# Optimization experiments

Measured on AMD Instinct MI355X. Metric: run time of the kernel, lower is better.

The kernel has to match this reference:

```python
import jax, jax.numpy as jnp
import numpy as np

DEPTH = 3

def _rx(theta):
    c, s = jnp.cos(theta / 2), jnp.sin(theta / 2)
    return jnp.stack([jnp.stack([c + 0j, -1j * s], -1),
                      jnp.stack([-1j * s, c + 0j], -1)], -2)

def _ry(theta):
    c, s = jnp.cos(theta / 2), jnp.sin(theta / 2)
    return jnp.stack([jnp.stack([c + 0j, -s + 0j], -1),
                      jnp.stack([s + 0j, c + 0j], -1)], -2)

def _rz(theta):
    e = jnp.exp(-0.5j * theta.astype(jnp.complex64))
    z = jnp.zeros_like(e)
    return jnp.stack([jnp.stack([e, z], -1),
                      jnp.stack([z, jnp.conj(e)], -1)], -2)

def _apply_1q(state, U, q):
    # state: (batch, 2,2,...,2); wire q lives on axis q+1. U: (2,2) or (batch,2,2)
    s = jnp.moveaxis(state, q + 1, -1)
    if U.ndim == 3:
        s = jnp.einsum('b...i,bji->b...j', s, U)
    else:
        s = jnp.einsum('...i,ji->...j', s, U)
    return jnp.moveaxis(s, -1, q + 1)

def _apply_cnot(state, c, t):
    s = jnp.moveaxis(state, (c + 1, t + 1), (-2, -1))
    s = jnp.concatenate([s[..., 0:1, :], s[..., 1:2, ::-1]], axis=-2)
    return jnp.moveaxis(s, (-2, -1), (c + 1, t + 1))

def _circuit(x, params):
    batch, n = x.shape
    depth = params.shape[0]
    state = jnp.zeros((batch,) + (2,) * n, jnp.complex64)
    state = state.at[(slice(None),) + (0,) * n].set(1.0)
    # data-encoding RX with per-sample angles
    for q in range(n):
        state = _apply_1q(state, _rx(x[:, q].astype(jnp.complex64).real), q)
    for l in range(depth):
        for q in range(n):
            state = _apply_1q(state, _rx(params[l, q, 0]), q)
            state = _apply_1q(state, _ry(params[l, q, 1]), q)
            state = _apply_1q(state, _rz(params[l, q, 2]), q)
        for q in range(n - 1):
            state = _apply_cnot(state, q, q + 1)
        state = _apply_cnot(state, n - 1, 0)
    probs = state.real ** 2 + state.imag ** 2  # (batch, 2,...,2)
    exps = []
    for w in range(n):
        p = jnp.moveaxis(probs, w + 1, 1).reshape(batch, 2, -1).sum(-1)
        exps.append(p[:, 0] - p[:, 1])  # <Z_w> = P(0) - P(1)
    return jnp.stack(exps, axis=1)


def setup_inputs() -> dict:
    key = jax.random.key(0)
    k1, k2 = jax.random.split(key)
    batch, n = 128, 14
    x = jax.random.normal(k1, (batch, n), dtype=jnp.float32)
    params = jax.random.normal(k2, (DEPTH, n, 3), dtype=jnp.float32)
    return {"x": x, "params": params}


def reference(x, params):
    return _circuit(x, params)
```

## Files before the change

kernel.cpp:

```cpp
#include <hip/hip_runtime.h>

namespace {

constexpr int NQ      = 14;
constexpr int NSTATES = 1 << NQ;
constexpr int BLOCK   = 1024;
constexpr int NWAVES  = BLOCK / 64;

constexpr unsigned cparity(unsigned x){ x^=x>>8; x^=x>>4; x^=x>>2; x^=x>>1; return x&1u; }

struct Mat { unsigned row[NQ]; unsigned col[NQ]; };

constexpr Mat m_after(int nr){
  Mat m{};
  for(int p=0;p<NQ;++p){ m.row[p]=1u<<p; m.col[p]=1u<<p; }
  for(int l=0;l<nr;++l)
    for(int q=0;q<NQ;++q){
      int cq=(q==NQ-1)?NQ-1:q, tq=(q==NQ-1)?0:q+1;
      int Pc=NQ-1-cq, Pt=NQ-1-tq;
      m.row[Pt]^=m.row[Pc]; m.col[Pc]^=m.col[Pt];
    }
  return m;
}

constexpr Mat M1=m_after(1), M2=m_after(2), M3=m_after(3);
constexpr unsigned amask(int q){ return M1.col[NQ-1-q]; }
constexpr unsigned arow (int q){ return M1.row[NQ-1-q]; }
constexpr unsigned bmask(int q){ return M2.col[NQ-1-q]; }
constexpr unsigned brow (int q){ return M2.row[NQ-1-q]; }

constexpr int rank_of(const unsigned* v, int n){
  unsigned a[24]{};
  for(int i=0;i<n;++i) a[i]=v[i];
  int r=0;
  for(int bit=15;bit>=0;--bit){
    int p=-1;
    for(int i=r;i<n;++i){ if((a[i]>>bit)&1){ p=i; break; } }
    if(p<0) continue;
    unsigned t=a[r]; a[r]=a[p]; a[p]=t;
    for(int i=0;i<n;++i) if(i!=r && ((a[i]>>bit)&1)) a[i]^=a[r];
    ++r;
  }
  return r;
}

struct Plan {
  unsigned A[14], B[14], C[14];
  int BlaneGi[6]; unsigned BlanePi4[6];
  int BregGi[4];  unsigned BregEps[4];
  int CregGi[4];  unsigned CregEps[4];
  int ClaneGi[4]; unsigned ClaneEps[4];
  unsigned EJ4[14], ET[14];
};

constexpr Plan make_plan(){
  Plan P{};
  for(int t=0;t<14;++t) P.A[t]=amask(t);
  for(int t=0;t<4;++t){ P.B[t]=amask(10+t); P.BregGi[t]=10+t; }
  bool used[14]{}; int picked[14]{}; int np=0;
  {
    unsigned cur[20]{}; int nc=0;
    for(int t=0;t<4;++t) cur[nc++]=P.B[t];
    for(int q=0;q<14 && np<10;++q){
      cur[nc]=bmask(q);
      if(rank_of(cur,nc+1)==nc+1){ ++nc; picked[np++]=q; used[q]=true; }
    }
  }
  for(int i=0;i<6;++i){ P.B[4+i]=bmask(picked[i]); P.BlaneGi[i]=14+picked[i]; }
  int wq[4]{}, un[4]{}; int nu=0;
  for(int i=0;i<4;++i){ wq[i]=picked[6+i]; P.B[10+i]=bmask(wq[i]); P.CregGi[i]=14+wq[i]; }
  for(int q=0;q<14;++q) if(!used[q]) un[nu++]=q;
  for(int i=0;i<4;++i) P.ClaneGi[i]=14+un[i];
  for(int i=0;i<4;++i){ unsigned m=0;
    for(int t=0;t<10;++t) m |= cparity(arow(10+i)&P.B[4+t])<<t;
    P.BregEps[i]=m; }
  for(int i=0;i<6;++i){ unsigned m=0;
    for(int t=0;t<4;++t) m |= cparity(brow(picked[i])&P.B[t])<<t;
    P.BlanePi4[i]=m; }
  for(int t=0;t<4;++t) P.C[t]=bmask(wq[t]);
  for(int t=0;t<4;++t) P.C[4+t]=bmask(un[t]);
  {
    unsigned cc[20]{}; int n=0;
    for(int t=0;t<8;++t) cc[n++]=P.C[t];
    int pos=8;
    for(int p=0;p<14 && pos<14;++p){
      cc[n]=1u<<p;
      if(rank_of(cc,n+1)==n+1){ P.C[pos]=1u<<p; ++n; ++pos; }
    }
  }
  for(int i=0;i<4;++i){ unsigned m=0;
    for(int t=0;t<10;++t) m |= cparity(brow(wq[i])&P.C[4+t])<<t;
    P.CregEps[i]=m; }
  for(int i=0;i<4;++i){ unsigned m=0;
    for(int t=0;t<10;++t){ if(t==i) continue; m |= cparity(brow(un[i])&P.C[4+t])<<t; }
    P.ClaneEps[i]=m; }
  for(int w=0;w<14;++w){
    unsigned R=M3.row[NQ-1-w]; unsigned mj=0, mt=0;
    for(int t=0;t<4;++t)  mj |= cparity(R&P.C[t])<<t;
    for(int t=0;t<10;++t) mt |= cparity(R&P.C[4+t])<<t;
    P.EJ4[w]=mj; P.ET[w]=mt;
  }
  return P;
}

constexpr Plan PL = make_plan();
static_assert(rank_of(PL.A,14)==14, "phase A map not bijective");
static_assert(rank_of(PL.B,14)==14, "phase B map not bijective");
static_assert(rank_of(PL.C,14)==14, "phase C map not bijective");

struct Inv { unsigned col[NQ]; };
constexpr Inv inv_basis(const unsigned* bas){
  unsigned vec[NQ]{}, cmb[NQ]{}; bool used[NQ]{}; int pivk[NQ]{};
  for(int k=0;k<NQ;++k){ vec[k]=bas[k]; cmb[k]=1u<<k; }
  for(int b=0;b<NQ;++b){
    int p=-1;
    for(int k=0;k<NQ;++k) if(!used[k] && ((vec[k]>>b)&1)){ p=k; break; }
    used[p]=true; pivk[b]=p;
    for(int k=0;k<NQ;++k) if(k!=p && ((vec[k]>>b)&1)){ vec[k]^=vec[p]; cmb[k]^=cmb[p]; }
  }
  Inv R{};
  for(int b=0;b<NQ;++b) R.col[b]=cmb[pivk[b]];
  return R;
}
constexpr bool check_inv(const unsigned* bas, const Inv& iv){
  for(int p=0;p<NQ;++p){
    unsigned s=0;
    for(int k=0;k<NQ;++k) if((iv.col[p]>>k)&1) s^=bas[k];
    if(s != (1u<<p)) return false;
  }
  return true;
}
constexpr Inv IA = inv_basis(PL.A), IB = inv_basis(PL.B), IC = inv_basis(PL.C);
static_assert(check_inv(PL.A, IA), "IA");
static_assert(check_inv(PL.B, IB), "IB");
static_assert(check_inv(PL.C, IC), "IC");

struct Trans { unsigned t[NQ]; };
constexpr Trans trans_phys(const Inv& iv){
  Trans T{};
  for(int p=0;p<NQ;++p) T.t[p]=iv.col[p];
  return T;
}
constexpr Trans trans_of(const unsigned* cur, const Inv& iv){
  Trans T{};
  for(int k=0;k<NQ;++k){
    unsigned c=0;
    for(int p=0;p<NQ;++p) if((cur[k]>>p)&1) c^=iv.col[p];
    T.t[k]=c;
  }
  return T;
}
constexpr Trans T_PA = trans_phys(IA);
constexpr Trans T_AB = trans_of(PL.A, IB);
constexpr Trans T_BC = trans_of(PL.B, IC);

struct CJ { unsigned v[16]; };
constexpr CJ mk_cj(const Trans& T){
  CJ c{};
  for(int j=0;j<16;++j){
    unsigned s=0;
    for(int b=0;b<4;++b) if((j>>b)&1) s^=T.t[b];
    c.v[j]=s;
  }
  return c;
}
constexpr CJ CJ_PA=mk_cj(T_PA), CJ_AB=mk_cj(T_AB), CJ_BC=mk_cj(T_BC);

__device__ __forceinline__ float2 cmul2(float2 a, float2 b){
  return make_float2(fmaf(a.x, b.x, -(a.y * b.y)),
                     fmaf(a.x, b.y,  a.y * b.x));
}
__device__ __forceinline__ float2 cfma2(float2 a, float2 b, float2 c){
  return make_float2(fmaf(a.x, b.x, fmaf(-a.y, b.y, c.x)),
                     fmaf(a.x, b.y, fmaf( a.y, b.x, c.y)));
}
__device__ __forceinline__ float2 sel2f(bool c, float2 x, float2 y){
  return make_float2(c ? x.x : y.x, c ? x.y : y.y);
}

struct GC { float2 u00,u01,u10,u11; };
__device__ __forceinline__ GC load_gc(const float2* __restrict__ g){
  const float4* p = reinterpret_cast<const float4*>(g);
  float4 q0=p[0], q1=p[1];
  GC c;
  c.u00=make_float2(q0.x,q0.y); c.u01=make_float2(q0.z,q0.w);
  c.u10=make_float2(q1.x,q1.y); c.u11=make_float2(q1.z,q1.w);
  return c;
}

template<int CTRL>
__device__ __forceinline__ int dpp(int x){
  return __builtin_amdgcn_update_dpp(0, x, CTRL, 0xF, 0xF, true);
}
__device__ __forceinline__ int x32(int x, unsigned lane){
  auto r = __builtin_amdgcn_permlane32_swap((unsigned)x, (unsigned)x, false, false);
  return (lane & 32u) ? (int)r[0] : (int)r[1];
}
template<int K>
__device__ __forceinline__ float2 xpart(float2 v, unsigned lane){
  int x0=__float_as_int(v.x), x1=__float_as_int(v.y);
  int y0, y1;
  if constexpr (K==0){ y0=dpp<0xB1>(x0);  y1=dpp<0xB1>(x1); }
  else if constexpr (K==1){ y0=dpp<0x4E>(x0);  y1=dpp<0x4E>(x1); }
  else if constexpr (K==2){
    y0=__builtin_amdgcn_ds_swizzle(x0,0x101F);
    y1=__builtin_amdgcn_ds_swizzle(x1,0x101F);
  }
  else if constexpr (K==3){ y0=dpp<0x128>(x0); y1=dpp<0x128>(x1); }
  else if constexpr (K==4){
    y0=__builtin_amdgcn_ds_swizzle(x0,0x401F);
    y1=__builtin_amdgcn_ds_swizzle(x1,0x401F);
  }
  else { y0=x32(x0,lane); y1=x32(x1,lane); }
  return make_float2(__int_as_float(y0), __int_as_float(y1));
}

template<int BIT>
__device__ __forceinline__ void reg_gate(float2 (&a)[16], const GC& c, bool eps){
  float2 m00=sel2f(eps,c.u11,c.u00), m01=sel2f(eps,c.u10,c.u01);
  float2 m10=sel2f(eps,c.u01,c.u10), m11=sel2f(eps,c.u00,c.u11);
#pragma unroll
  for(int v=0; v<16; ++v){
    if(!((v>>BIT)&1)){
      int w = v | (1<<BIT);
      float2 a0=a[v], a1=a[w];
      a[v] = cfma2(m01, a1, cmul2(m00, a0));
      a[w] = cfma2(m11, a1, cmul2(m10, a0));
    }
  }
}

template<int XK, unsigned PI4>
__device__ __forceinline__ void lane_gate(float2 (&a)[16], const GC& c, bool sel, unsigned lane){
  float2 ka0=sel2f(sel,c.u11,c.u00), kb0=sel2f(sel,c.u10,c.u01);
  float2 ka1=sel2f(sel,c.u00,c.u11), kb1=sel2f(sel,c.u01,c.u10);
  float2 th[16];
#pragma unroll
  for(int j=0;j<16;++j) th[j] = xpart<XK>(a[j], lane);
#pragma unroll
  for(int j=0;j<16;++j){
    bool pi = (__builtin_popcount(PI4 & (unsigned)j) & 1) != 0;
    float2 ka = pi?ka1:ka0, kb = pi?kb1:kb0;
    a[j] = cfma2(kb, th[j], cmul2(ka, a[j]));
  }
}

__device__ __forceinline__ unsigned nb_of(unsigned tid, const unsigned (&t)[NQ]){
  unsigned s=0;
#pragma unroll
  for(int k=0;k<10;++k) s ^= t[4+k] & (0u-((tid>>k)&1u));
  return s;
}

__device__ __forceinline__ void scatter16(float2* __restrict__ st, const float2 (&a)[16],
                                          unsigned nb, const CJ& cj){
#pragma unroll
  for(int j=0;j<16;++j){
    unsigned d = nb ^ cj.v[j];
    st[d + (d>>4)] = a[j];
  }
}

__global__ __launch_bounds__(BLOCK, 4) void qsim_kernel(
    const float* __restrict__ x,
    const float* __restrict__ prm,
    float* __restrict__ out)
{
  __shared__ float2 st[BLOCK*17];
  __shared__ alignas(16) float2 Utab[28*4];
  __shared__ float2 l0c[NQ][2];
  __shared__ float  red[NWAVES][NQ];

  const int b = blockIdx.x;
  const unsigned tid = threadIdx.x;
  const unsigned lane = tid & 63u;

  if(tid < 28){
    int t = tid;
    int l = 1 + t/NQ, q = t % NQ;
    float ax=prm[(l*NQ+q)*3+0], ay=prm[(l*NQ+q)*3+1], az=prm[(l*NQ+q)*3+2];
    float cx,sx,cy,sy,cz,sz;
    sincosf(0.5f*ax,&sx,&cx); sincosf(0.5f*ay,&sy,&cy); sincosf(0.5f*az,&sz,&cz);
    float2 M00=make_float2(cy*cx, sy*sx),  M01=make_float2(-sy*cx,-cy*sx);
    float2 M10=make_float2(sy*cx,-cy*sx),  M11=make_float2(cy*cx,-sy*sx);
    float2 ez =make_float2(cz,-sz), ezc=make_float2(cz,sz);
    float2* U = &Utab[t*4];
    U[0]=cmul2(ez,M00); U[1]=cmul2(ez,M01);
    U[2]=cmul2(ezc,M10); U[3]=cmul2(ezc,M11);
  }
  if(tid < NQ){
    int q = tid;
    float ax = prm[q*3+0] + x[b*NQ+q];
    float ay = prm[q*3+1], az = prm[q*3+2];
    float cx,sx,cy,sy,cz,sz;
    sincosf(0.5f*ax,&sx,&cx); sincosf(0.5f*ay,&sy,&cy); sincosf(0.5f*az,&sz,&cz);
    l0c[q][0] = cmul2(make_float2(cz,-sz), make_float2(cy*cx,  sy*sx));
    l0c[q][1] = cmul2(make_float2(cz, sz), make_float2(sy*cx, -cy*sx));
  }
  __syncthreads();

  {
    float2 p01 = cmul2(l0c[0][(tid>>9)&1],  l0c[1][(tid>>8)&1]);
    float2 p23 = cmul2(l0c[2][(tid>>7)&1],  l0c[3][(tid>>6)&1]);
    float2 p45 = cmul2(l0c[4][(tid>>5)&1],  l0c[5][(tid>>4)&1]);
    float2 p67 = cmul2(l0c[6][(tid>>3)&1],  l0c[7][(tid>>2)&1]);
    float2 p89 = cmul2(l0c[8][(tid>>1)&1],  l0c[9][tid&1]);
    float2 Pk  = cmul2(cmul2(cmul2(p01,p23), cmul2(p45,p67)), p89);
    float2 t2[2], t4[4];
    t2[0]=cmul2(Pk,l0c[10][0]); t2[1]=cmul2(Pk,l0c[10][1]);
#pragma unroll
    for(int i=0;i<2;++i){ t4[2*i]=cmul2(t2[i],l0c[11][0]); t4[2*i+1]=cmul2(t2[i],l0c[11][1]); }
    float2 a[16];
#pragma unroll
    for(int j=0;j<16;++j){
      a[j] = cmul2(cmul2(t4[j>>2], l0c[12][(j>>1)&1]), l0c[13][j&1]);
    }
    scatter16(st, a, nb_of(tid, T_PA.t), CJ_PA);
  }
  __syncthreads();

  {
    float2 a[16];
    const int rb = (int)tid*17;
#pragma unroll
    for(int j=0;j<16;++j) a[j] = st[rb + j];
    reg_gate<0>(a, load_gc(Utab+0*4), false);
    reg_gate<1>(a, load_gc(Utab+1*4), false);
    reg_gate<2>(a, load_gc(Utab+2*4), false);
    reg_gate<3>(a, load_gc(Utab+3*4), false);
    lane_gate<0,0u>(a, load_gc(Utab+4*4), (tid&1)!=0,  lane);
    lane_gate<1,0u>(a, load_gc(Utab+5*4), (tid&2)!=0,  lane);
    lane_gate<2,0u>(a, load_gc(Utab+6*4), (tid&4)!=0,  lane);
    lane_gate<3,0u>(a, load_gc(Utab+7*4), (tid&8)!=0,  lane);
    lane_gate<4,0u>(a, load_gc(Utab+8*4), (tid&16)!=0, lane);
    lane_gate<5,0u>(a, load_gc(Utab+9*4), (tid&32)!=0, lane);
    __syncthreads();
    scatter16(st, a, nb_of(tid, T_AB.t), CJ_AB);
  }
  __syncthreads();

  {
    float2 a[16];
    const int rb = (int)tid*17;
#pragma unroll
    for(int j=0;j<16;++j) a[j] = st[rb + j];
    reg_gate<0>(a, load_gc(Utab+PL.BregGi[0]*4), (__builtin_popcount(PL.BregEps[0]&tid)&1)!=0);
    reg_gate<1>(a, load_gc(Utab+PL.BregGi[1]*4), (__builtin_popcount(PL.BregEps[1]&tid)&1)!=0);
    reg_gate<2>(a, load_gc(Utab+PL.BregGi[2]*4), (__builtin_popcount(PL.BregEps[2]&tid)&1)!=0);
    reg_gate<3>(a, load_gc(Utab+PL.BregGi[3]*4), (__builtin_popcount(PL.BregEps[3]&tid)&1)!=0);
    lane_gate<0,PL.BlanePi4[0]>(a, load_gc(Utab+PL.BlaneGi[0]*4), (tid&1)!=0,  lane);
    lane_gate<1,PL.BlanePi4[1]>(a, load_gc(Utab+PL.BlaneGi[1]*4), (tid&2)!=0,  lane);
    lane_gate<2,PL.BlanePi4[2]>(a, load_gc(Utab+PL.BlaneGi[2]*4), (tid&4)!=0,  lane);
    lane_gate<3,PL.BlanePi4[3]>(a, load_gc(Utab+PL.BlaneGi[3]*4), (tid&8)!=0,  lane);
    lane_gate<4,PL.BlanePi4[4]>(a, load_gc(Utab+PL.BlaneGi[4]*4), (tid&16)!=0, lane);
    lane_gate<5,PL.BlanePi4[5]>(a, load_gc(Utab+PL.BlaneGi[5]*4), (tid&32)!=0, lane);
    __syncthreads();
    scatter16(st, a, nb_of(tid, T_BC.t), CJ_BC);
  }
  __syncthreads();

  {
    float2 a[16];
    const int rb = (int)tid*17;
#pragma unroll
    for(int j=0;j<16;++j) a[j] = st[rb + j];
    reg_gate<0>(a, load_gc(Utab+PL.CregGi[0]*4), (__builtin_popcount(PL.CregEps[0]&tid)&1)!=0);
    reg_gate<1>(a, load_gc(Utab+PL.CregGi[1]*4), (__builtin_popcount(PL.CregEps[1]&tid)&1)!=0);
    reg_gate<2>(a, load_gc(Utab+PL.CregGi[2]*4), (__builtin_popcount(PL.CregEps[2]&tid)&1)!=0);
    reg_gate<3>(a, load_gc(Utab+PL.CregGi[3]*4), (__builtin_popcount(PL.CregEps[3]&tid)&1)!=0);
    lane_gate<0,0u>(a, load_gc(Utab+PL.ClaneGi[0]*4),
        (((tid&1u)!=0) != ((__builtin_popcount(PL.ClaneEps[0]&tid)&1)!=0)), lane);
    lane_gate<1,0u>(a, load_gc(Utab+PL.ClaneGi[1]*4),
        (((tid&2u)!=0) != ((__builtin_popcount(PL.ClaneEps[1]&tid)&1)!=0)), lane);
    lane_gate<2,0u>(a, load_gc(Utab+PL.ClaneGi[2]*4),
        (((tid&4u)!=0) != ((__builtin_popcount(PL.ClaneEps[2]&tid)&1)!=0)), lane);
    lane_gate<3,0u>(a, load_gc(Utab+PL.ClaneGi[3]*4),
        (((tid&8u)!=0) != ((__builtin_popcount(PL.ClaneEps[3]&tid)&1)!=0)), lane);

    float p[16];
#pragma unroll
    for(int j=0;j<16;++j) p[j] = a[j].x*a[j].x + a[j].y*a[j].y;
#pragma unroll
    for(int bstep=1; bstep<16; bstep<<=1){
#pragma unroll
      for(int j=0;j<16;++j){
        if(!(j & bstep)){
          float u = p[j], v = p[j|bstep];
          p[j] = u + v;
          p[j|bstep] = u - v;
        }
      }
    }
    const int wave = tid >> 6;
#pragma unroll
    for(int w=0;w<NQ;++w){
      float v = (__builtin_popcount(PL.ET[w]&tid)&1) ? -p[PL.EJ4[w]] : p[PL.EJ4[w]];
#pragma unroll
      for(int off=32; off>0; off>>=1) v += __shfl_down(v, off, 64);
      if(lane==0) red[wave][w]=v;
    }
    __syncthreads();
    if(tid < NQ){
      float s=0.f;
#pragma unroll
      for(int wv=0; wv<NWAVES; ++wv) s += red[wv][tid];
      out[b*NQ + tid] = s;
    }
  }
}

}

extern "C" void kernel_launch(void* const* d_in, const int* in_sizes, int n_in,
                              void* d_out, int out_size, void* d_ws, size_t ws_size,
                              hipStream_t stream) {
  const float* x   = (const float*)d_in[0];
  const float* prm = (const float*)d_in[1];
  float* out = (float*)d_out;
  const int batch = in_sizes[0] / NQ;
  qsim_kernel<<<batch, BLOCK, 0, stream>>>(x, prm, out);
}
```

Measured before the change: 37.97 us.

## Store state in LDS as packed fp16, use permlane16 swap and DPP reductions

The shared-memory state buffer changes from float2 to packed half2 (cvt_pkrtz on write, convert back on read). This halves LDS footprint and bandwidth per scatter and gather, and the smaller buffer could also let more blocks fit per CU. The lane-16 exchange now uses permlane16_swap instead of ds_swizzle where the builtin exists. The wave reduction is rewritten from shfl_down to a DPP, swizzle and permlane butterfly. Storing amplitudes in fp16 between stages lowers precision and risks accuracy tolerance failures.

```diff
diff --git a/kernel.cpp b/kernel.cpp
--- a/kernel.cpp
+++ b/kernel.cpp
@@ -166,6 +166,16 @@
 }
 constexpr CJ CJ_PA=mk_cj(T_PA), CJ_AB=mk_cj(T_AB), CJ_BC=mk_cj(T_BC);
 
+using h2v = __fp16 __attribute__((ext_vector_type(2)));
+__device__ __forceinline__ unsigned pack_h2(float2 a){
+  h2v h = __builtin_amdgcn_cvt_pkrtz(a.x, a.y);
+  return __builtin_bit_cast(unsigned, h);
+}
+__device__ __forceinline__ float2 unpack_h2(unsigned u){
+  h2v h = __builtin_bit_cast(h2v, u);
+  return make_float2((float)h[0], (float)h[1]);
+}
+
 __device__ __forceinline__ float2 cmul2(float2 a, float2 b){
   return make_float2(fmaf(a.x, b.x, -(a.y * b.y)),
                      fmaf(a.x, b.y,  a.y * b.x));
@@ -195,6 +205,14 @@
 __device__ __forceinline__ int x32(int x, unsigned lane){
   auto r = __builtin_amdgcn_permlane32_swap((unsigned)x, (unsigned)x, false, false);
   return (lane & 32u) ? (int)r[0] : (int)r[1];
+}
+__device__ __forceinline__ int x16(int x, unsigned lane){
+#if __has_builtin(__builtin_amdgcn_permlane16_swap)
+  auto r = __builtin_amdgcn_permlane16_swap((unsigned)x, (unsigned)x, false, false);
+  return (lane & 16u) ? (int)r[0] : (int)r[1];
+#else
+  return __builtin_amdgcn_ds_swizzle(x, 0x401F);
+#endif
 }
 template<int K>
 __device__ __forceinline__ float2 xpart(float2 v, unsigned lane){
@@ -207,10 +225,7 @@
     y1=__builtin_amdgcn_ds_swizzle(x1,0x101F);
   }
   else if constexpr (K==3){ y0=dpp<0x128>(x0); y1=dpp<0x128>(x1); }
-  else if constexpr (K==4){
-    y0=__builtin_amdgcn_ds_swizzle(x0,0x401F);
-    y1=__builtin_amdgcn_ds_swizzle(x1,0x401F);
-  }
+  else if constexpr (K==4){ y0=x16(x0,lane); y1=x16(x1,lane); }
   else { y0=x32(x0,lane); y1=x32(x1,lane); }
   return make_float2(__int_as_float(y0), __int_as_float(y1));
 }
@@ -245,6 +260,16 @@
   }
 }
 
+__device__ __forceinline__ float xsum64(float v, unsigned lane){
+  v += __int_as_float(dpp<0xB1>(__float_as_int(v)));
+  v += __int_as_float(dpp<0x4E>(__float_as_int(v)));
+  v += __int_as_float(__builtin_amdgcn_ds_swizzle(__float_as_int(v),0x101F));
+  v += __int_as_float(dpp<0x128>(__float_as_int(v)));
+  v += __int_as_float(x16(__float_as_int(v), lane));
+  v += __int_as_float(x32(__float_as_int(v), lane));
+  return v;
+}
+
 __device__ __forceinline__ unsigned nb_of(unsigned tid, const unsigned (&t)[NQ]){
   unsigned s=0;
 #pragma unroll
@@ -252,12 +277,12 @@
   return s;
 }
 
-__device__ __forceinline__ void scatter16(float2* __restrict__ st, const float2 (&a)[16],
+__device__ __forceinline__ void scatter16(unsigned* __restrict__ st, const float2 (&a)[16],
                                           unsigned nb, const CJ& cj){
 #pragma unroll
   for(int j=0;j<16;++j){
     unsigned d = nb ^ cj.v[j];
-    st[d + (d>>4)] = a[j];
+    st[d + (d>>4)] = pack_h2(a[j]);
   }
 }
 
@@ -266,7 +291,7 @@
     const float* __restrict__ prm,
     float* __restrict__ out)
 {
-  __shared__ float2 st[BLOCK*17];
+  __shared__ unsigned st[BLOCK*17];
   __shared__ alignas(16) float2 Utab[28*4];
   __shared__ float2 l0c[NQ][2];
   __shared__ float  red[NWAVES][NQ];
@@ -323,7 +348,7 @@
     float2 a[16];
     const int rb = (int)tid*17;
 #pragma unroll
-    for(int j=0;j<16;++j) a[j] = st[rb + j];
+    for(int j=0;j<16;++j) a[j] = unpack_h2(st[rb + j]);
     reg_gate<0>(a, load_gc(Utab+0*4), false);
     reg_gate<1>(a, load_gc(Utab+1*4), false);
     reg_gate<2>(a, load_gc(Utab+2*4), false);
@@ -343,7 +368,7 @@
     float2 a[16];
     const int rb = (int)tid*17;
 #pragma unroll
-    for(int j=0;j<16;++j) a[j] = st[rb + j];
+    for(int j=0;j<16;++j) a[j] = unpack_h2(st[rb + j]);
     reg_gate<0>(a, load_gc(Utab+PL.BregGi[0]*4), (__builtin_popcount(PL.BregEps[0]&tid)&1)!=0);
     reg_gate<1>(a, load_gc(Utab+PL.BregGi[1]*4), (__builtin_popcount(PL.BregEps[1]&tid)&1)!=0);
     reg_gate<2>(a, load_gc(Utab+PL.BregGi[2]*4), (__builtin_popcount(PL.BregEps[2]&tid)&1)!=0);
@@ -363,7 +388,7 @@
     float2 a[16];
     const int rb = (int)tid*17;
 #pragma unroll
-    for(int j=0;j<16;++j) a[j] = st[rb + j];
+    for(int j=0;j<16;++j) a[j] = unpack_h2(st[rb + j]);
     reg_gate<0>(a, load_gc(Utab+PL.CregGi[0]*4), (__builtin_popcount(PL.CregEps[0]&tid)&1)!=0);
     reg_gate<1>(a, load_gc(Utab+PL.CregGi[1]*4), (__builtin_popcount(PL.CregEps[1]&tid)&1)!=0);
     reg_gate<2>(a, load_gc(Utab+PL.CregGi[2]*4), (__builtin_popcount(PL.CregEps[2]&tid)&1)!=0);
@@ -395,8 +420,7 @@
 #pragma unroll
     for(int w=0;w<NQ;++w){
       float v = (__builtin_popcount(PL.ET[w]&tid)&1) ? -p[PL.EJ4[w]] : p[PL.EJ4[w]];
-#pragma unroll
-      for(int off=32; off>0; off>>=1) v += __shfl_down(v, off, 64);
+      v = xsum64(v, lane);
       if(lane==0) red[wave][w]=v;
     }
     __syncthreads();
```

Result: slower. 43.56 us (+14.7%).

## Simulate state vector in packed half2 with fp16 FMA gates

Applied to the files above, without the earlier changes.

Stores the amplitudes as packed half2 (re, im) in registers and shared memory, and applies gates with packed fp16 FMAs. The gate coefficients are pre-expanded into duplicated half2 pairs, with a halfword swap for the cross terms. This halves LDS traffic and footprint and shrinks register pressure. Lane shuffles move one dword per amplitude instead of two. It also replaces the shfl_down reduction with a DPP/swizzle/permlane butterfly and uses permlane16_swap when it is available. The risk is fp16 precision loss across about 60 gate applications, which could exceed the accuracy tolerance.

```diff
diff --git a/kernel.cpp b/kernel.cpp
--- a/kernel.cpp
+++ b/kernel.cpp
@@ -1,4 +1,5 @@
 #include <hip/hip_runtime.h>
+#include <hip/hip_fp16.h>
 
 namespace {
 
@@ -166,83 +167,102 @@
 }
 constexpr CJ CJ_PA=mk_cj(T_PA), CJ_AB=mk_cj(T_AB), CJ_BC=mk_cj(T_BC);
 
+__device__ __forceinline__ __half2 H2(unsigned u){ return __builtin_bit_cast(__half2, u); }
+__device__ __forceinline__ unsigned U32(__half2 h){ return __builtin_bit_cast(unsigned, h); }
+__device__ __forceinline__ unsigned hswap(unsigned u){ return __builtin_amdgcn_alignbit(u, u, 16); }
+
 __device__ __forceinline__ float2 cmul2(float2 a, float2 b){
   return make_float2(fmaf(a.x, b.x, -(a.y * b.y)),
                      fmaf(a.x, b.y,  a.y * b.x));
 }
-__device__ __forceinline__ float2 cfma2(float2 a, float2 b, float2 c){
-  return make_float2(fmaf(a.x, b.x, fmaf(-a.y, b.y, c.x)),
-                     fmaf(a.x, b.y, fmaf( a.y, b.x, c.y)));
-}
-__device__ __forceinline__ float2 sel2f(bool c, float2 x, float2 y){
-  return make_float2(c ? x.x : y.x, c ? x.y : y.y);
-}
-
-struct GC { float2 u00,u01,u10,u11; };
-__device__ __forceinline__ GC load_gc(const float2* __restrict__ g){
-  const float4* p = reinterpret_cast<const float4*>(g);
-  float4 q0=p[0], q1=p[1];
+
+struct GC { unsigned e[8]; };
+__device__ __forceinline__ GC load_gc(const unsigned* __restrict__ g){
+  const uint4* p = reinterpret_cast<const uint4*>(g);
+  uint4 q0=p[0], q1=p[1];
   GC c;
-  c.u00=make_float2(q0.x,q0.y); c.u01=make_float2(q0.z,q0.w);
-  c.u10=make_float2(q1.x,q1.y); c.u11=make_float2(q1.z,q1.w);
+  c.e[0]=q0.x; c.e[1]=q0.y; c.e[2]=q0.z; c.e[3]=q0.w;
+  c.e[4]=q1.x; c.e[5]=q1.y; c.e[6]=q1.z; c.e[7]=q1.w;
   return c;
 }
 
+__device__ __forceinline__ void gpair(__half2& r0, __half2& r1, const unsigned (&m)[8],
+                                      __half2 a0, __half2 a1){
+  __half2 a0s = H2(hswap(U32(a0))), a1s = H2(hswap(U32(a1)));
+  r0 = __hfma2(H2(m[0]),a0, __hfma2(H2(m[1]),a0s, __hfma2(H2(m[2]),a1, __hmul2(H2(m[3]),a1s))));
+  r1 = __hfma2(H2(m[4]),a0, __hfma2(H2(m[5]),a0s, __hfma2(H2(m[6]),a1, __hmul2(H2(m[7]),a1s))));
+}
+
 template<int CTRL>
-__device__ __forceinline__ int dpp(int x){
-  return __builtin_amdgcn_update_dpp(0, x, CTRL, 0xF, 0xF, true);
-}
-__device__ __forceinline__ int x32(int x, unsigned lane){
-  auto r = __builtin_amdgcn_permlane32_swap((unsigned)x, (unsigned)x, false, false);
-  return (lane & 32u) ? (int)r[0] : (int)r[1];
+__device__ __forceinline__ unsigned dppu(unsigned x){
+  return (unsigned)__builtin_amdgcn_update_dpp(0, (int)x, CTRL, 0xF, 0xF, true);
+}
+__device__ __forceinline__ unsigned x32u(unsigned x, unsigned lane){
+  auto r = __builtin_amdgcn_permlane32_swap(x, x, false, false);
+  return (lane & 32u) ? (unsigned)r[0] : (unsigned)r[1];
+}
+__device__ __forceinline__ unsigned x16u(unsigned x, unsigned lane){
+#if __has_builtin(__builtin_amdgcn_permlane16_swap)
+  auto r = __builtin_amdgcn_permlane16_swap(x, x, false, false);
+  return (lane & 16u) ? (unsigned)r[0] : (unsigned)r[1];
+#else
+  return (unsigned)__builtin_amdgcn_ds_swizzle((int)x, 0x401F);
+#endif
 }
 template<int K>
-__device__ __forceinline__ float2 xpart(float2 v, unsigned lane){
-  int x0=__float_as_int(v.x), x1=__float_as_int(v.y);
-  int y0, y1;
-  if constexpr (K==0){ y0=dpp<0xB1>(x0);  y1=dpp<0xB1>(x1); }
-  else if constexpr (K==1){ y0=dpp<0x4E>(x0);  y1=dpp<0x4E>(x1); }
-  else if constexpr (K==2){
-    y0=__builtin_amdgcn_ds_swizzle(x0,0x101F);
-    y1=__builtin_amdgcn_ds_swizzle(x1,0x101F);
-  }
-  else if constexpr (K==3){ y0=dpp<0x128>(x0); y1=dpp<0x128>(x1); }
-  else if constexpr (K==4){
-    y0=__builtin_amdgcn_ds_swizzle(x0,0x401F);
-    y1=__builtin_amdgcn_ds_swizzle(x1,0x401F);
-  }
-  else { y0=x32(x0,lane); y1=x32(x1,lane); }
-  return make_float2(__int_as_float(y0), __int_as_float(y1));
+__device__ __forceinline__ unsigned xpart_u32(unsigned x, unsigned lane){
+  if constexpr (K==0) return dppu<0xB1>(x);
+  else if constexpr (K==1) return dppu<0x4E>(x);
+  else if constexpr (K==2) return (unsigned)__builtin_amdgcn_ds_swizzle((int)x,0x101F);
+  else if constexpr (K==3) return dppu<0x128>(x);
+  else if constexpr (K==4) return x16u(x,lane);
+  else return x32u(x,lane);
 }
 
 template<int BIT>
-__device__ __forceinline__ void reg_gate(float2 (&a)[16], const GC& c, bool eps){
-  float2 m00=sel2f(eps,c.u11,c.u00), m01=sel2f(eps,c.u10,c.u01);
-  float2 m10=sel2f(eps,c.u01,c.u10), m11=sel2f(eps,c.u00,c.u11);
+__device__ __forceinline__ void reg_gate(__half2 (&a)[16], const GC& c, bool eps){
+  unsigned m[8];
+#pragma unroll
+  for(int i=0;i<8;++i) m[i] = eps ? c.e[i^6] : c.e[i];
 #pragma unroll
   for(int v=0; v<16; ++v){
     if(!((v>>BIT)&1)){
       int w = v | (1<<BIT);
-      float2 a0=a[v], a1=a[w];
-      a[v] = cfma2(m01, a1, cmul2(m00, a0));
-      a[w] = cfma2(m11, a1, cmul2(m10, a0));
+      __half2 n0, n1;
+      gpair(n0, n1, m, a[v], a[w]);
+      a[v]=n0; a[w]=n1;
     }
   }
 }
 
 template<int XK, unsigned PI4>
-__device__ __forceinline__ void lane_gate(float2 (&a)[16], const GC& c, bool sel, unsigned lane){
-  float2 ka0=sel2f(sel,c.u11,c.u00), kb0=sel2f(sel,c.u10,c.u01);
-  float2 ka1=sel2f(sel,c.u00,c.u11), kb1=sel2f(sel,c.u01,c.u10);
-  float2 th[16];
-#pragma unroll
-  for(int j=0;j<16;++j) th[j] = xpart<XK>(a[j], lane);
+__device__ __forceinline__ void lane_gate(__half2 (&a)[16], const GC& c, bool sel, unsigned lane){
+  unsigned ka0x = sel?c.e[6]:c.e[0], ka0n = sel?c.e[7]:c.e[1];
+  unsigned kb0x = sel?c.e[4]:c.e[2], kb0n = sel?c.e[5]:c.e[3];
+  unsigned ka1x = sel?c.e[0]:c.e[6], ka1n = sel?c.e[1]:c.e[7];
+  unsigned kb1x = sel?c.e[2]:c.e[4], kb1n = sel?c.e[3]:c.e[5];
+  unsigned th[16];
+#pragma unroll
+  for(int j=0;j<16;++j) th[j] = xpart_u32<XK>(U32(a[j]), lane);
 #pragma unroll
   for(int j=0;j<16;++j){
     bool pi = (__builtin_popcount(PI4 & (unsigned)j) & 1) != 0;
-    float2 ka = pi?ka1:ka0, kb = pi?kb1:kb0;
-    a[j] = cfma2(kb, th[j], cmul2(ka, a[j]));
-  }
+    unsigned kax = pi?ka1x:ka0x, kan = pi?ka1n:ka0n;
+    unsigned kbx = pi?kb1x:kb0x, kbn = pi?kb1n:kb0n;
+    __half2 as  = H2(hswap(U32(a[j])));
+    __half2 ths = H2(hswap(th[j]));
+    a[j] = __hfma2(H2(kax),a[j], __hfma2(H2(kan),as, __hfma2(H2(kbx),H2(th[j]), __hmul2(H2(kbn),ths))));
+  }
+}
+
+__device__ __forceinline__ float xsum64(float v, unsigned lane){
+  v += __int_as_float((int)dppu<0xB1>((unsigned)__float_as_int(v)));
+  v += __int_as_float((int)dppu<0x4E>((unsigned)__float_as_int(v)));
+  v += __int_as_float(__builtin_amdgcn_ds_swizzle(__float_as_int(v),0x101F));
+  v += __int_as_float((int)dppu<0x128>((unsigned)__float_as_int(v)));
+  v += __int_as_float((int)x16u((unsigned)__float_as_int(v), lane));
+  v += __int_as_float((int)x32u((unsigned)__float_as_int(v), lane));
+  return v;
 }
 
 __device__ __forceinline__ unsigned nb_of(unsigned tid, const unsigned (&t)[NQ]){
@@ -252,12 +272,12 @@
   return s;
 }
 
-__device__ __forceinline__ void scatter16(float2* __restrict__ st, const float2 (&a)[16],
+__device__ __forceinline__ void scatter16(unsigned* __restrict__ st, const __half2 (&a)[16],
                                           unsigned nb, const CJ& cj){
 #pragma unroll
   for(int j=0;j<16;++j){
     unsigned d = nb ^ cj.v[j];
-    st[d + (d>>4)] = a[j];
+    st[d + (d>>4)] = U32(a[j]);
   }
 }
 
@@ -266,8 +286,8 @@
     const float* __restrict__ prm,
     float* __restrict__ out)
 {
-  __shared__ float2 st[BLOCK*17];
-  __shared__ alignas(16) float2 Utab[28*4];
+  __shared__ unsigned st[BLOCK*17];
+  __shared__ alignas(16) unsigned Utab[28*8];
   __shared__ float2 l0c[NQ][2];
   __shared__ float  red[NWAVES][NQ];
 
@@ -284,9 +304,12 @@
     float2 M00=make_float2(cy*cx, sy*sx),  M01=make_float2(-sy*cx,-cy*sx);
     float2 M10=make_float2(sy*cx,-cy*sx),  M11=make_float2(cy*cx,-sy*sx);
     float2 ez =make_float2(cz,-sz), ezc=make_float2(cz,sz);
-    float2* U = &Utab[t*4];
-    U[0]=cmul2(ez,M00); U[1]=cmul2(ez,M01);
-    U[2]=cmul2(ezc,M10); U[3]=cmul2(ezc,M11);
+    float2 U00=cmul2(ez,M00), U01=cmul2(ez,M01), U10=cmul2(ezc,M10), U11=cmul2(ezc,M11);
+    unsigned* U = &Utab[t*8];
+    U[0]=U32(__floats2half2_rn( U00.x,U00.x)); U[1]=U32(__floats2half2_rn(-U00.y,U00.y));
+    U[2]=U32(__floats2half2_rn( U01.x,U01.x)); U[3]=U32(__floats2half2_rn(-U01.y,U01.y));
+    U[4]=U32(__floats2half2_rn( U10.x,U10.x)); U[5]=U32(__floats2half2_rn(-U10.y,U10.y));
+    U[6]=U32(__floats2half2_rn( U11.x,U11.x)); U[7]=U32(__floats2half2_rn(-U11.y,U11.y));
   }
   if(tid < NQ){
     int q = tid;
@@ -310,76 +333,80 @@
     t2[0]=cmul2(Pk,l0c[10][0]); t2[1]=cmul2(Pk,l0c[10][1]);
 #pragma unroll
     for(int i=0;i<2;++i){ t4[2*i]=cmul2(t2[i],l0c[11][0]); t4[2*i+1]=cmul2(t2[i],l0c[11][1]); }
-    float2 a[16];
+    __half2 a[16];
 #pragma unroll
     for(int j=0;j<16;++j){
-      a[j] = cmul2(cmul2(t4[j>>2], l0c[12][(j>>1)&1]), l0c[13][j&1]);
+      float2 v = cmul2(cmul2(t4[j>>2], l0c[12][(j>>1)&1]), l0c[13][j&1]);
+      a[j] = __floats2half2_rn(v.x, v.y);
     }
     scatter16(st, a, nb_of(tid, T_PA.t), CJ_PA);
   }
   __syncthreads();
 
   {
-    float2 a[16];
+    __half2 a[16];
     const int rb = (int)tid*17;
 #pragma unroll
-    for(int j=0;j<16;++j) a[j] = st[rb + j];
-    reg_gate<0>(a, load_gc(Utab+0*4), false);
-    reg_gate<1>(a, load_gc(Utab+1*4), false);
-    reg_gate<2>(a, load_gc(Utab+2*4), false);
-    reg_gate<3>(a, load_gc(Utab+3*4), false);
-    lane_gate<0,0u>(a, load_gc(Utab+4*4), (tid&1)!=0,  lane);
-    lane_gate<1,0u>(a, load_gc(Utab+5*4), (tid&2)!=0,  lane);
-    lane_gate<2,0u>(a, load_gc(Utab+6*4), (tid&4)!=0,  lane);
-    lane_gate<3,0u>(a, load_gc(Utab+7*4), (tid&8)!=0,  lane);
-    lane_gate<4,0u>(a, load_gc(Utab+8*4), (tid&16)!=0, lane);
-    lane_gate<5,0u>(a, load_gc(Utab+9*4), (tid&32)!=0, lane);
+    for(int j=0;j<16;++j) a[j] = H2(st[rb + j]);
+    reg_gate<0>(a, load_gc(Utab+0*8), false);
+    reg_gate<1>(a, load_gc(Utab+1*8), false);
+    reg_gate<2>(a, load_gc(Utab+2*8), false);
+    reg_gate<3>(a, load_gc(Utab+3*8), false);
+    lane_gate<0,0u>(a, load_gc(Utab+4*8), (tid&1)!=0,  lane);
+    lane_gate<1,0u>(a, load_gc(Utab+5*8), (tid&2)!=0,  lane);
+    lane_gate<2,0u>(a, load_gc(Utab+6*8), (tid&4)!=0,  lane);
+    lane_gate<3,0u>(a, load_gc(Utab+7*8), (tid&8)!=0,  lane);
+    lane_gate<4,0u>(a, load_gc(Utab+8*8), (tid&16)!=0, lane);
+    lane_gate<5,0u>(a, load_gc(Utab+9*8), (tid&32)!=0, lane);
     __syncthreads();
     scatter16(st, a, nb_of(tid, T_AB.t), CJ_AB);
   }
   __syncthreads();
 
   {
-    float2 a[16];
+    __half2 a[16];
     const int rb = (int)tid*17;
 #pragma unroll
-    for(int j=0;j<16;++j) a[j] = st[rb + j];
-    reg_gate<0>(a, load_gc(Utab+PL.BregGi[0]*4), (__builtin_popcount(PL.BregEps[0]&tid)&1)!=0);
-    reg_gate<1>(a, load_gc(Utab+PL.BregGi[1]*4), (__builtin_popcount(PL.BregEps[1]&tid)&1)!=0);
-    reg_gate<2>(a, load_gc(Utab+PL.BregGi[2]*4), (__builtin_popcount(PL.BregEps[2]&tid)&1)!=0);
-    reg_gate<3>(a, load_gc(Utab+PL.BregGi[3]*4), (__builtin_popcount(PL.BregEps[3]&tid)&1)!=0);
-    lane_gate<0,PL.BlanePi4[0]>(a, load_gc(Utab+PL.BlaneGi[0]*4), (tid&1)!=0,  lane);
-    lane_gate<1,PL.BlanePi4[1]>(a, load_gc(Utab+PL.BlaneGi[1]*4), (tid&2)!=0,  lane);
-    lane_gate<2,PL.BlanePi4[2]>(a, load_gc(Utab+PL.BlaneGi[2]*4), (tid&4)!=0,  lane);
-    lane_gate<3,PL.BlanePi4[3]>(a, load_gc(Utab+PL.BlaneGi[3]*4), (tid&8)!=0,  lane);
-    lane_gate<4,PL.BlanePi4[4]>(a, load_gc(Utab+PL.BlaneGi[4]*4), (tid&16)!=0, lane);
-    lane_gate<5,PL.BlanePi4[5]>(a, load_gc(Utab+PL.BlaneGi[5]*4), (tid&32)!=0, lane);
+    for(int j=0;j<16;++j) a[j] = H2(st[rb + j]);
+    reg_gate<0>(a, load_gc(Utab+PL.BregGi[0]*8), (__builtin_popcount(PL.BregEps[0]&tid)&1)!=0);
+    reg_gate<1>(a, load_gc(Utab+PL.BregGi[1]*8), (__builtin_popcount(PL.BregEps[1]&tid)&1)!=0);
+    reg_gate<2>(a, load_gc(Utab+PL.BregGi[2]*8), (__builtin_popcount(PL.BregEps[2]&tid)&1)!=0);
+    reg_gate<3>(a, load_gc(Utab+PL.BregGi[3]*8), (__builtin_popcount(PL.BregEps[3]&tid)&1)!=0);
+    lane_gate<0,PL.BlanePi4[0]>(a, load_gc(Utab+PL.BlaneGi[0]*8), (tid&1)!=0,  lane);
+    lane_gate<1,PL.BlanePi4[1]>(a, load_gc(Utab+PL.BlaneGi[1]*8), (tid&2)!=0,  lane);
+    lane_gate<2,PL.BlanePi4[2]>(a, load_gc(Utab+PL.BlaneGi[2]*8), (tid&4)!=0,  lane);
+    lane_gate<3,PL.BlanePi4[3]>(a, load_gc(Utab+PL.BlaneGi[3]*8), (tid&8)!=0,  lane);
+    lane_gate<4,PL.BlanePi4[4]>(a, load_gc(Utab+PL.BlaneGi[4]*8), (tid&16)!=0, lane);
+    lane_gate<5,PL.BlanePi4[5]>(a, load_gc(Utab+PL.BlaneGi[5]*8), (tid&32)!=0, lane);
     __syncthreads();
     scatter16(st, a, nb_of(tid, T_BC.t), CJ_BC);
   }
   __syncthreads();
 
   {
-    float2 a[16];
+    __half2 a[16];
     const int rb = (int)tid*17;
 #pragma unroll
-    for(int j=0;j<16;++j) a[j] = st[rb + j];
-    reg_gate<0>(a, load_gc(Utab+PL.CregGi[0]*4), (__builtin_popcount(PL.CregEps[0]&tid)&1)!=0);
-    reg_gate<1>(a, load_gc(Utab+PL.CregGi[1]*4), (__builtin_popcount(PL.CregEps[1]&tid)&1)!=0);
-    reg_gate<2>(a, load_gc(Utab+PL.CregGi[2]*4), (__builtin_popcount(PL.CregEps[2]&tid)&1)!=0);
-    reg_gate<3>(a, load_gc(Utab+PL.CregGi[3]*4), (__builtin_popcount(PL.CregEps[3]&tid)&1)!=0);
-    lane_gate<0,0u>(a, load_gc(Utab+PL.ClaneGi[0]*4),
+    for(int j=0;j<16;++j) a[j] = H2(st[rb + j]);
+    reg_gate<0>(a, load_gc(Utab+PL.CregGi[0]*8), (__builtin_popcount(PL.CregEps[0]&tid)&1)!=0);
+    reg_gate<1>(a, load_gc(Utab+PL.CregGi[1]*8), (__builtin_popcount(PL.CregEps[1]&tid)&1)!=0);
+    reg_gate<2>(a, load_gc(Utab+PL.CregGi[2]*8), (__builtin_popcount(PL.CregEps[2]&tid)&1)!=0);
+    reg_gate<3>(a, load_gc(Utab+PL.CregGi[3]*8), (__builtin_popcount(PL.CregEps[3]&tid)&1)!=0);
+    lane_gate<0,0u>(a, load_gc(Utab+PL.ClaneGi[0]*8),
         (((tid&1u)!=0) != ((__builtin_popcount(PL.ClaneEps[0]&tid)&1)!=0)), lane);
-    lane_gate<1,0u>(a, load_gc(Utab+PL.ClaneGi[1]*4),
+    lane_gate<1,0u>(a, load_gc(Utab+PL.ClaneGi[1]*8),
         (((tid&2u)!=0) != ((__builtin_popcount(PL.ClaneEps[1]&tid)&1)!=0)), lane);
-    lane_gate<2,0u>(a, load_gc(Utab+PL.ClaneGi[2]*4),
+    lane_gate<2,0u>(a, load_gc(Utab+PL.ClaneGi[2]*8),
         (((tid&4u)!=0) != ((__builtin_popcount(PL.ClaneEps[2]&tid)&1)!=0)), lane);
-    lane_gate<3,0u>(a, load_gc(Utab+PL.ClaneGi[3]*4),
+    lane_gate<3,0u>(a, load_gc(Utab+PL.ClaneGi[3]*8),
         (((tid&8u)!=0) != ((__builtin_popcount(PL.ClaneEps[3]&tid)&1)!=0)), lane);
 
     float p[16];
 #pragma unroll
-    for(int j=0;j<16;++j) p[j] = a[j].x*a[j].x + a[j].y*a[j].y;
+    for(int j=0;j<16;++j){
+      float re = __low2float(a[j]), im = __high2float(a[j]);
+      p[j] = fmaf(re, re, im*im);
+    }
 #pragma unroll
     for(int bstep=1; bstep<16; bstep<<=1){
 #pragma unroll
@@ -395,8 +422,7 @@
 #pragma unroll
     for(int w=0;w<NQ;++w){
       float v = (__builtin_popcount(PL.ET[w]&tid)&1) ? -p[PL.EJ4[w]] : p[PL.EJ4[w]];
-#pragma unroll
-      for(int off=32; off>0; off>>=1) v += __shfl_down(v, off, 64);
+      v = xsum64(v, lane);
       if(lane==0) red[wave][w]=v;
     }
     __syncthreads();
```

New measurement: 37.00 us, median of 2. 2.6% less time.
